# Performance work log

Hardware: AMD Instinct MI355X
Metric: run time of the kernel (lower is better)

The kernel has to match this reference:

```python
import jax, jax.numpy as jnp
import numpy as np

B, S, C, D, P = 32, 720, 2048, 256, 96
LATENT_DIMS = [512, 128, 32]  # enc_in // 4 ** k, e_layers=3
NL = 3
ALPHA = 0.1
EPS = 1e-5


def _ln(x, g, b, eps=1e-5):
    m = jnp.mean(x, axis=-1, keepdims=True)
    v = jnp.var(x, axis=-1, keepdims=True)
    return (x - m) * jax.lax.rsqrt(v + eps) * g + b


def _cov_loss(skips, lam=ALPHA, eps=EPS):
    total = jnp.zeros((), dtype=jnp.float32)
    for x in skips[1:]:
        b, c, d = x.shape
        xr = x.reshape(b * c, d)
        xc = (xr - jnp.mean(xr, axis=0, keepdims=True)) / (jnp.std(xr, axis=0, ddof=1, keepdims=True) + eps)
        cov = xc.T @ xc / (b * c - 1) + eps * jnp.eye(d, dtype=x.dtype)
        total = total - jnp.linalg.slogdet(cov)[1] / d
    return lam * total / (len(skips) - 1)


def setup_inputs() -> dict:
    key = jax.random.key(0)
    ks = jax.random.split(key, 16)
    w = lambda k, shp: (jax.random.normal(k, shp, dtype=jnp.float32) * 0.02)
    inp = {
        'x_enc': jax.random.normal(ks[0], (B, S, C), dtype=jnp.float32),
        'x_mark_enc': jnp.zeros((B, S, 4), dtype=jnp.float32),
        'x_dec': jnp.zeros((B, P, C), dtype=jnp.float32),
        'x_mark_dec': jnp.zeros((B, P, 4), dtype=jnp.float32),
        'in_w': w(ks[1], (S, D)), 'in_b': jnp.zeros((D,), jnp.float32),
        'lq0': jax.random.normal(ks[2], (LATENT_DIMS[0], D), dtype=jnp.float32),
        'lq1': jax.random.normal(ks[3], (LATENT_DIMS[1], D), dtype=jnp.float32),
        'lq2': jax.random.normal(ks[4], (LATENT_DIMS[2], D), dtype=jnp.float32),
        'down_w': w(ks[5], (NL, 4, D, D)), 'down_b': jnp.zeros((NL, 4, D), jnp.float32),
        'down_ln': jnp.stack([jnp.ones((NL, D)), jnp.zeros((NL, D))], axis=1).astype(jnp.float32),
        'pred_w': w(ks[6], (D, D)), 'pred_b': jnp.zeros((D,), jnp.float32),
        'up_w': w(ks[7], (NL, 4, D, D)), 'up_b': jnp.zeros((NL, 4, D), jnp.float32),
        'up_ln': jnp.stack([jnp.ones((NL, D)), jnp.zeros((NL, D))], axis=1).astype(jnp.float32),
        'out_w': w(ks[8], (D, P)), 'out_b': jnp.zeros((P,), jnp.float32),
    }
    return inp


def _forward(x_enc, in_w, in_b, lqs, down_w, down_b, down_ln,
             pred_w, pred_b, up_w, up_b, up_ln, out_w, out_b):
    # instance norm over time
    means = jnp.mean(x_enc, axis=1, keepdims=True)            # [B,1,C]
    xc = x_enc - means
    stdev = jnp.sqrt(jnp.var(xc, axis=1, keepdims=True) + 1e-5)
    xn = xc / stdev
    # transpose + Linear(seq_len -> d_model): [B,C,D]
    h = jnp.einsum('bsc,sd->bcd', xn, in_w) + in_b

    scale = 1.0 / jnp.sqrt(jnp.asarray(D, dtype=h.dtype))
    skips = [h]
    x = h
    for i in range(NL):
        Wq, Wk, Wv, Wo = down_w[i]
        bq, bk, bv, bo = down_b[i]
        q = lqs[i] @ Wq + bq                                  # [Lq,D] shared over batch
        k = x @ Wk + bk                                       # [B,L,D]
        v = x @ Wv + bv
        attn = jax.nn.softmax(jnp.einsum('qd,bld->bql', q, k) * scale, axis=-1)
        o = jnp.einsum('bql,bld->bqd', attn, v) @ Wo + bo
        x = _ln(o, down_ln[i, 0], down_ln[i, 1])
        skips.append(x)

    cov = _cov_loss(skips)

    x = x @ pred_w + pred_b                                   # bottom [B,32,D]
    queries = skips[::-1][1:]                                 # [128-skip, 512-skip, base]
    for i, qin in enumerate(queries):
        Wq, Wk, Wv, Wo = up_w[i]
        bq, bk, bv, bo = up_b[i]
        q = qin @ Wq + bq                                     # [B,Lq,D]
        k = x @ Wk + bk                                       # [B,Lk,D]
        v = x @ Wv + bv
        attn = jax.nn.softmax(jnp.einsum('bqd,bld->bql', q, k) * scale, axis=-1)
        o = jnp.einsum('bql,bld->bqd', attn, v) @ Wo + bo
        x = _ln(o + qin, up_ln[i, 0], up_ln[i, 1])

    dec = (x + h) @ out_w + out_b                             # [B,C,P]
    dec = jnp.transpose(dec, (0, 2, 1))                       # [B,P,C]
    dec = dec * stdev[:, 0, :][:, None, :] + means[:, 0, :][:, None, :]
    return dec, cov


def reference(x_enc, x_mark_enc, x_dec, x_mark_dec, in_w, in_b, lq0, lq1, lq2,
              down_w, down_b, down_ln, pred_w, pred_b, up_w, up_b, up_ln, out_w, out_b):
    return _forward(x_enc, in_w, in_b, (lq0, lq1, lq2), down_w, down_b, down_ln,
                    pred_w, pred_b, up_w, up_b, up_ln, out_w, out_b)
```

## Files before the change

kernel.cpp:

```cpp
#include <hip/hip_runtime.h>
#include <hip/hip_bf16.h>
#include <math.h>

#define CDIV(a, b) (((a) + (b) - 1) / (b))
typedef long long ll;
typedef unsigned short ushort_t;

constexpr int Bn = 32;
constexpr int Sn = 720;
constexpr int SnP = 736;
constexpr int Cn = 2048;
constexpr int Dn = 256;
constexpr int Pn = 96;

typedef __attribute__((ext_vector_type(8))) short bf16x8;
typedef __attribute__((ext_vector_type(4))) float f32x4;

__device__ inline ushort_t rne1(float x) {
  unsigned u = __float_as_uint(x);
  u = (u + 0x7fffu + ((u >> 16) & 1u)) >> 16;
  return (ushort_t)u;
}
__device__ inline float b2f(ushort_t u) { return __uint_as_float(((unsigned)u) << 16); }

__device__ inline void gl_lds16(const void* g, void* l) {
  __builtin_amdgcn_global_load_lds(
      (const __attribute__((address_space(1))) void*)g,
      (__attribute__((address_space(3))) void*)l, 16, 0, 0);
}

__global__ void instnorm_stats(const float* __restrict__ x,
                               float* __restrict__ mean, float* __restrict__ stdev) {
  int c = blockIdx.x * 256 + threadIdx.x;
  int b = blockIdx.y;
  const float* p = x + (ll)b * Sn * Cn + c;
  float s = 0.f, q = 0.f;
  for (int t = 0; t < Sn; ++t) {
    float v = p[(ll)t * Cn];
    s += v; q += v * v;
  }
  float m = s / (float)Sn;
  float var = q / (float)Sn - m * m;
  var = fmaxf(var, 0.f);
  mean[b * Cn + c] = m;
  stdev[b * Cn + c] = sqrtf(var + 1e-5f);
}

__global__ void normT_kernel(const float* __restrict__ X, ushort_t* __restrict__ D,
                             const float* __restrict__ mean,
                             const float* __restrict__ stdev) {
  int b = blockIdx.z;
  __shared__ float tl[32][33];
  int t = threadIdx.x;
  int tx = t & 31, ty = t >> 5;
  int s0 = blockIdx.y * 32, c0 = blockIdx.x * 32;
#pragma unroll
  for (int e = 0; e < 4; ++e) {
    int s = s0 + ty + 8 * e;
    tl[ty + 8 * e][tx] = (s < Sn) ? X[((ll)b * Sn + s) * Cn + c0 + tx] : 0.f;
  }
  __syncthreads();
#pragma unroll
  for (int e = 0; e < 4; ++e) {
    int c = c0 + ty + 8 * e, s = s0 + tx;
    if (s < SnP) {
      float mu = mean[b * Cn + c], sd = stdev[b * Cn + c];
      float v = (s < Sn) ? (tl[tx][ty + 8 * e] - mu) / sd : 0.f;
      D[((ll)b * Cn + c) * SnP + s] = rne1(v);
    }
  }
}

__global__ void cvtT_kernel(const float* __restrict__ S, ushort_t* __restrict__ D,
                            int K, int N, int KP) {
  int z = blockIdx.z;
  S += (ll)z * K * N;
  D += (ll)z * N * KP;
  __shared__ float tl[32][33];
  int t = threadIdx.x;
  int tx = t & 31, ty = t >> 5;
  int k0 = blockIdx.y * 32, n0 = blockIdx.x * 32;
#pragma unroll
  for (int e = 0; e < 4; ++e) {
    int k = k0 + ty + 8 * e;
    tl[ty + 8 * e][tx] = (k < K && n0 + tx < N) ? S[(ll)k * N + n0 + tx] : 0.f;
  }
  __syncthreads();
#pragma unroll
  for (int e = 0; e < 4; ++e) {
    int n = n0 + ty + 8 * e, kk = k0 + tx;
    if (n < N && kk < KP) D[(ll)n * KP + kk] = rne1(tl[tx][ty + 8 * e]);
  }
}

__global__ void cvt_bf(const float* __restrict__ S, ushort_t* __restrict__ D, int n) {
  int i = blockIdx.x * 256 + threadIdx.x;
  if (i < n) D[i] = rne1(S[i]);
}

template <int MODE>
__global__ __launch_bounds__(256) void gemm_bf(
    const ushort_t* __restrict__ A, const ushort_t* __restrict__ B,
    int M, int N, int K, int lda, int ldb, ll sA, ll sB,
    const float* __restrict__ bias, float alpha,
    float* __restrict__ Cf, int ldcf, ll sCf,
    ushort_t* __restrict__ Cb, int ldcb, ll sCb) {
  int g = blockIdx.z;
  A += (ll)g * sA;
  B += (ll)g * sB;
  if (MODE & 1) Cf += (ll)g * sCf;
  if (MODE & 6) Cb += (ll)g * sCb;
  __shared__ ushort_t lds_ab[2][128][32];
  int t = threadIdx.x;
  int m0 = blockIdx.y * 128, n0 = blockIdx.x * 128;
  int w = t >> 6, lane = t & 63;
  int wm = (w >> 1) * 64, wn = (w & 1) * 64;
  int lrow = lane & 15, kq = lane >> 4;
  int srow = lane >> 2, skcol = (lane & 3) * 8;
  f32x4 acc[4][4] = {};
  for (int k0 = 0; k0 < K; k0 += 32) {
#pragma unroll
    for (int cc = 0; cc < 4; ++cc) {
      int c = w * 4 + cc;
      int tile = c >> 3, rb = (c & 7) * 16;
      int row = rb + srow;
      const ushort_t* src;
      if (tile == 0) {
        int gm = min(m0 + row, M - 1);
        src = &A[(ll)gm * lda + k0 + skcol];
      } else {
        int gn = min(n0 + row, N - 1);
        src = &B[(ll)gn * ldb + k0 + skcol];
      }
      gl_lds16(src, &lds_ab[tile][rb][0]);
    }
    __syncthreads();
    bf16x8 af[4], bfr[4];
#pragma unroll
    for (int i = 0; i < 4; ++i)
      af[i] = *reinterpret_cast<const bf16x8*>(&lds_ab[0][wm + i * 16 + lrow][kq * 8]);
#pragma unroll
    for (int j = 0; j < 4; ++j)
      bfr[j] = *reinterpret_cast<const bf16x8*>(&lds_ab[1][wn + j * 16 + lrow][kq * 8]);
#pragma unroll
    for (int i = 0; i < 4; ++i)
#pragma unroll
      for (int j = 0; j < 4; ++j)
        acc[i][j] = __builtin_amdgcn_mfma_f32_16x16x32_bf16(af[i], bfr[j],
                                                            acc[i][j], 0, 0, 0);
    __syncthreads();
  }
#pragma unroll
  for (int i = 0; i < 4; ++i) {
    int mb = m0 + wm + i * 16 + kq * 4;
    if (mb >= M) continue;
#pragma unroll
    for (int j = 0; j < 4; ++j) {
      int c = n0 + wn + j * 16 + lrow;
      if (c >= N) continue;
      float bv = bias ? bias[c] : 0.f;
#pragma unroll
      for (int reg = 0; reg < 4; ++reg) {
        int m = mb + reg;
        float v = acc[i][j][reg] * alpha + bv;
        if (MODE & 1) Cf[(ll)m * ldcf + c] = v;
        if (MODE & 2) Cb[(ll)m * ldcb + c] = rne1(v);
        if (MODE & 4) Cb[(ll)c * ldcb + m] = rne1(v);
      }
    }
  }
}

__device__ inline float blk_reduce(float v, volatile float* sh, int op) {
  int lane = threadIdx.x & 63, w = threadIdx.x >> 6;
#pragma unroll
  for (int off = 32; off > 0; off >>= 1) {
    float o = __shfl_down(v, off, 64);
    v = op ? fmaxf(v, o) : (v + o);
  }
  __syncthreads();
  if (lane == 0) sh[w] = v;
  __syncthreads();
  float r = op ? fmaxf(fmaxf(sh[0], sh[1]), fmaxf(sh[2], sh[3]))
               : (sh[0] + sh[1] + sh[2] + sh[3]);
  return r;
}

template <int LL>
__global__ void softmax_bf(const float* __restrict__ S, ushort_t* __restrict__ P) {
  constexpr int NE = (LL + 255) / 256;
  __shared__ float sh[4];
  ll row = blockIdx.x;
  const float* p = S + row * (ll)LL;
  ushort_t* q = P + row * (ll)LL;
  int t = threadIdx.x;
  float e[NE];
  float mx = -INFINITY;
#pragma unroll
  for (int k = 0; k < NE; ++k) {
    int i = t + k * 256;
    if (i < LL) { e[k] = p[i]; mx = fmaxf(mx, e[k]); }
  }
  mx = blk_reduce(mx, sh, 1);
  float sum = 0.f;
#pragma unroll
  for (int k = 0; k < NE; ++k) {
    int i = t + k * 256;
    if (i < LL) { e[k] = __expf(e[k] - mx); sum += e[k]; }
  }
  sum = blk_reduce(sum, sh, 0);
  float inv = 1.f / sum;
#pragma unroll
  for (int k = 0; k < NE; ++k) {
    int i = t + k * 256;
    if (i < LL) q[i] = rne1(e[k] * inv);
  }
}

__global__ void ln_kernel(const float* __restrict__ X, const ushort_t* __restrict__ RESb,
                          float* __restrict__ Yf, ushort_t* __restrict__ Yb, int postadd,
                          const float* __restrict__ gamma, const float* __restrict__ beta) {
  __shared__ float sh[4];
  ll row = blockIdx.x;
  int t = threadIdx.x;
  float r = RESb ? b2f(RESb[row * Dn + t]) : 0.f;
  float v = X[row * Dn + t] + r;
  float m = blk_reduce(v, sh, 0) * (1.f / (float)Dn);
  float d = v - m;
  float var = blk_reduce(d * d, sh, 0) * (1.f / (float)Dn);
  float y = d * rsqrtf(var + 1e-5f) * gamma[t] + beta[t];
  if (Yf) Yf[row * Dn + t] = y;
  if (Yb) Yb[row * Dn + t] = rne1(y + (postadd ? r : 0.f));
}

__global__ void colstat_partial(const float* __restrict__ X, double* __restrict__ part,
                                int nrows) {
  int blk = blockIdx.x, t = threadIdx.x;
  int chunk = CDIV(nrows, 256);
  int r0 = blk * chunk, r1 = min(nrows, r0 + chunk);
  double s = 0.0, q = 0.0;
  for (int r = r0; r < r1; ++r) {
    double v = (double)X[(ll)r * Dn + t];
    s += v; q += v * v;
  }
  part[blk * 512 + t] = s;
  part[blk * 512 + 256 + t] = q;
}

__global__ void colstat_final(const double* __restrict__ part, float* __restrict__ cmean,
                              float* __restrict__ cistd, int nrows) {
  int t = threadIdx.x;
  double s = 0.0, q = 0.0;
  for (int b = 0; b < 256; ++b) {
    s += part[b * 512 + t];
    q += part[b * 512 + 256 + t];
  }
  double m = s / (double)nrows;
  double var = (q - (double)nrows * m * m) / (double)(nrows - 1);
  var = fmax(var, 0.0);
  cmean[t] = (float)m;
  cistd[t] = (float)(1.0 / (sqrt(var) + 1e-5));
}

__global__ __launch_bounds__(256) void cov_gram(const float* __restrict__ X,
                                                const float* __restrict__ cmean,
                                                const float* __restrict__ cistd,
                                                double* __restrict__ part, int nr) {
  __shared__ double Am[32][33];
  __shared__ double Bq[32][33];
  __shared__ float cmA[32], ciA[32], cmB[32], ciB[32];
  int tile = blockIdx.x;
  int mi = 0;
  while (tile >= mi + 1) { tile -= mi + 1; ++mi; }
  int nj = tile;
  int m0 = mi * 32, n0 = nj * 32;
  int z = blockIdx.y;
  int t = threadIdx.x, tx = t & 31, ty = t >> 5;
  if (t < 32) {
    cmA[t] = cmean[m0 + t]; ciA[t] = cistd[m0 + t];
    cmB[t] = cmean[n0 + t]; ciB[t] = cistd[n0 + t];
  }
  __syncthreads();
  int chunk = nr >> 4;
  int kbeg = z * chunk, kend = kbeg + chunk;
  double acc[4] = {0.0, 0.0, 0.0, 0.0};
  for (int k0 = kbeg; k0 < kend; k0 += 32) {
#pragma unroll
    for (int e = 0; e < 4; ++e) {
      int idx = t + e * 256;
      int kk = idx >> 5, mm = idx & 31;
      float xa = X[(ll)(k0 + kk) * Dn + m0 + mm];
      float xb = X[(ll)(k0 + kk) * Dn + n0 + mm];
      Am[kk][mm] = (double)((xa - cmA[mm]) * ciA[mm]);
      Bq[kk][mm] = (double)((xb - cmB[mm]) * ciB[mm]);
    }
    __syncthreads();
#pragma unroll 8
    for (int kk = 0; kk < 32; ++kk) {
      double bv = Bq[kk][tx];
#pragma unroll
      for (int r = 0; r < 4; ++r)
        acc[r] += Am[kk][ty + 8 * r] * bv;
    }
    __syncthreads();
  }
#pragma unroll
  for (int r = 0; r < 4; ++r) {
    int m = m0 + ty + 8 * r, n = n0 + tx;
    part[(ll)z * 65536 + m * 256 + n] = acc[r];
  }
}

__global__ void cov_reduce(const double* __restrict__ part, double* __restrict__ Cd,
                           double inv) {
  int tile = blockIdx.x;
  int mi = 0;
  while (tile >= mi + 1) { tile -= mi + 1; ++mi; }
  int nj = tile;
  int t = threadIdx.x;
#pragma unroll
  for (int e = 0; e < 4; ++e) {
    int idx = t + e * 256;
    int rr = idx >> 5, cc = idx & 31;
    int m = mi * 32 + rr, n = nj * 32 + cc;
    int off = m * 256 + n;
    double s = 0.0;
#pragma unroll
    for (int z = 0; z < 16; ++z) s += part[(ll)z * 65536 + off];
    Cd[off] = s * inv + ((m == n) ? 1e-5 : 0.0);
  }
}

__global__ __launch_bounds__(256) void chol_step_a(double* __restrict__ mats, int d0) {
  double* A = mats + (ll)blockIdx.x * 65536;
  __shared__ double D[32][33];
  __shared__ double dinv[32];
  int t = threadIdx.x;
  for (int e = t; e < 1024; e += 256) {
    int i = e >> 5, j = e & 31;
    D[i][j] = (j <= i) ? A[(ll)(d0 + i) * 256 + d0 + j] : 0.0;
  }
  __syncthreads();
  if (t < 32) {
    double x[32];
#pragma unroll
    for (int j = 0; j < 32; ++j) x[j] = D[t][j];
#pragma unroll
    for (int k = 0; k < 32; ++k) {
      double piv = fmax(__shfl(x[k], k, 64), 1e-300);
      double inv = 1.0 / sqrt(piv);
      double lrk = x[k] * inv;
      x[k] = lrk;
#pragma unroll
      for (int j = k + 1; j < 32; ++j) x[j] -= lrk * __shfl(lrk, j, 64);
    }
#pragma unroll
    for (int j = 0; j < 32; ++j) D[t][j] = x[j];
    dinv[t] = 1.0 / x[t];
  }
  __syncthreads();
  int r = d0 + 32 + t;
  if (r < 256) {
    double y[32];
#pragma unroll
    for (int j = 0; j < 32; ++j) y[j] = A[(ll)r * 256 + d0 + j];
#pragma unroll
    for (int j = 0; j < 32; ++j) {
      double s = y[j];
#pragma unroll
      for (int i = 0; i < j; ++i) s -= y[i] * D[j][i];
      y[j] = s * dinv[j];
    }
#pragma unroll
    for (int j = 0; j < 32; ++j) A[(ll)r * 256 + d0 + j] = y[j];
  }
  for (int e = t; e < 1024; e += 256)
    A[(ll)(d0 + (e >> 5)) * 256 + d0 + (e & 31)] = D[e >> 5][e & 31];
}

__global__ __launch_bounds__(256) void chol_step_b(double* __restrict__ mats, int d0) {
  double* A = mats + (ll)blockIdx.y * 65536;
  int tile = blockIdx.x;
  int i = 0;
  while (tile >= i + 1) { tile -= i + 1; ++i; }
  int j = tile;
  int ri = d0 + 32 + i * 32, rj = d0 + 32 + j * 32;
  __shared__ double Li[32][33];
  __shared__ double Lj[32][33];
  int t = threadIdx.x;
  for (int e = t; e < 1024; e += 256) {
    int rr = e >> 5, kk = e & 31;
    Li[rr][kk] = A[(ll)(ri + rr) * 256 + d0 + kk];
    Lj[rr][kk] = A[(ll)(rj + rr) * 256 + d0 + kk];
  }
  __syncthreads();
  for (int e = t; e < 1024; e += 256) {
    int rr = e >> 5, cc = e & 31;
    double s = 0.0;
#pragma unroll
    for (int k = 0; k < 32; ++k) s += Li[rr][k] * Lj[cc][k];
    A[(ll)(ri + rr) * 256 + rj + cc] -= s;
  }
}

__global__ void logdet_diag(const double* __restrict__ mats, double* __restrict__ ld) {
  __shared__ double sh[4];
  const double* A = mats + (ll)blockIdx.x * 65536;
  int t = threadIdx.x;
  double lg = log(A[(ll)t * 257]);
  int lane = t & 63, w = t >> 6;
#pragma unroll
  for (int off = 32; off > 0; off >>= 1) lg += __shfl_down(lg, off, 64);
  if (lane == 0) sh[w] = lg;
  __syncthreads();
  if (t == 0) ld[blockIdx.x] = 2.0 * (sh[0] + sh[1] + sh[2] + sh[3]);
}

__global__ void cov_final(const double* __restrict__ ld, float* __restrict__ outp) {
  outp[0] = (float)(-0.1 / (3.0 * 256.0) * (ld[0] + ld[1] + ld[2]));
}

__global__ __launch_bounds__(256) void out_mfma(
    const ushort_t* __restrict__ A, const ushort_t* __restrict__ B,
    const float* __restrict__ bias, const float* __restrict__ stdev,
    const float* __restrict__ mean, float* __restrict__ out) {
  constexpr int M = Bn * Cn, N = Pn, K = Dn;
  __shared__ ushort_t lds_ab[2][128][32];
  int t = threadIdx.x;
  int m0 = blockIdx.y * 128;
  int w = t >> 6, lane = t & 63;
  int wm = (w >> 1) * 64, wn = (w & 1) * 64;
  int lrow = lane & 15, kq = lane >> 4;
  int srow = lane >> 2, skcol = (lane & 3) * 8;
  f32x4 acc[4][4] = {};
  for (int k0 = 0; k0 < K; k0 += 32) {
#pragma unroll
    for (int cc = 0; cc < 4; ++cc) {
      int c = w * 4 + cc;
      int tile = c >> 3, rb = (c & 7) * 16;
      int row = rb + srow;
      const ushort_t* src;
      if (tile == 0) {
        src = &A[(ll)(m0 + row) * K + k0 + skcol];
      } else {
        int gn = min(row, N - 1);
        src = &B[(ll)gn * K + k0 + skcol];
      }
      gl_lds16(src, &lds_ab[tile][rb][0]);
    }
    __syncthreads();
    bf16x8 af[4], bfr[4];
#pragma unroll
    for (int i = 0; i < 4; ++i)
      af[i] = *reinterpret_cast<const bf16x8*>(&lds_ab[0][wm + i * 16 + lrow][kq * 8]);
#pragma unroll
    for (int j = 0; j < 4; ++j)
      bfr[j] = *reinterpret_cast<const bf16x8*>(&lds_ab[1][wn + j * 16 + lrow][kq * 8]);
#pragma unroll
    for (int i = 0; i < 4; ++i)
#pragma unroll
      for (int j = 0; j < 4; ++j)
        acc[i][j] = __builtin_amdgcn_mfma_f32_16x16x32_bf16(af[i], bfr[j],
                                                            acc[i][j], 0, 0, 0);
    __syncthreads();
  }
#pragma unroll
  for (int i = 0; i < 4; ++i) {
    int mb = m0 + wm + i * 16 + kq * 4;
#pragma unroll
    for (int j = 0; j < 4; ++j) {
      int p = wn + j * 16 + lrow;
      if (p >= N) continue;
      float bv = bias[p];
#pragma unroll
      for (int reg = 0; reg < 4; ++reg) {
        int m = mb + reg;
        int b = m >> 11, c = m & 2047;
        float v = acc[i][j][reg] + bv;
        out[((ll)(b * Pn + p)) * Cn + c] = v * stdev[m] + mean[m];
      }
    }
  }
}

extern "C" void kernel_launch(void* const* d_in, const int* in_sizes, int n_in,
                              void* d_out, int out_size, void* d_ws, size_t ws_size,
                              hipStream_t stream) {
  (void)in_sizes; (void)n_in; (void)out_size; (void)ws_size;
  const float* x_enc = (const float*)d_in[0];
  const float* in_w = (const float*)d_in[4];
  const float* in_b = (const float*)d_in[5];
  const float* lq[3] = {(const float*)d_in[6], (const float*)d_in[7],
                        (const float*)d_in[8]};
  const float* down_w = (const float*)d_in[9];
  const float* down_b = (const float*)d_in[10];
  const float* down_ln = (const float*)d_in[11];
  const float* pred_w = (const float*)d_in[12];
  const float* pred_b = (const float*)d_in[13];
  const float* up_w = (const float*)d_in[14];
  const float* up_b = (const float*)d_in[15];
  const float* up_ln = (const float*)d_in[16];
  const float* out_w = (const float*)d_in[17];
  const float* out_b = (const float*)d_in[18];
  float* out = (float*)d_out;

  float* ws = (float*)d_ws;
  size_t off = 0;
  auto alloc = [&](size_t n) {
    n = (n + 3) & ~(size_t)3;
    float* p = ws + off;
    off += n;
    return p;
  };
  float* mean = alloc((size_t)Bn * Cn);
  float* stdevv = alloc((size_t)Bn * Cn);
  float* cmean = alloc(256);
  float* cistd = alloc(256);
  double* part = (double*)alloc(256 * 512 * 2);
  double* ld = (double*)alloc(16);
  double* covd = (double*)alloc(3 * 65536 * 2);
  float* s1 = alloc((size_t)Bn * 512 * Dn);
  float* s2 = alloc((size_t)Bn * 128 * Dn);
  float* s3 = alloc((size_t)Bn * 32 * Dn);
  float* attn = alloc((size_t)Bn * 512 * 2048);
  float* sbuf = alloc((size_t)16777216);
  ushort_t* h_bf = (ushort_t*)alloc((size_t)Bn * Cn * Dn / 2);
  ushort_t* s1b = (ushort_t*)alloc((size_t)Bn * 512 * Dn / 2);
  ushort_t* s2b = (ushort_t*)alloc((size_t)Bn * 128 * Dn / 2);
  ushort_t* s3b = (ushort_t*)alloc((size_t)Bn * 32 * Dn / 2);
  ushort_t* xpb = (ushort_t*)alloc((size_t)Bn * 32 * Dn / 2);
  ushort_t* xu0b = (ushort_t*)alloc((size_t)Bn * 128 * Dn / 2);
  ushort_t* xu1b = (ushort_t*)alloc((size_t)Bn * 512 * Dn / 2);
  ushort_t* qd_b = (ushort_t*)alloc(512 * 256 / 2);
  ushort_t* lqb0 = (ushort_t*)alloc(512 * 256 / 2);
  ushort_t* lqb1 = (ushort_t*)alloc(128 * 256 / 2);
  ushort_t* lqb2 = (ushort_t*)alloc(32 * 256 / 2);
  ushort_t* in_wT = (ushort_t*)alloc(256 * SnP / 2);
  ushort_t* downT = (ushort_t*)alloc(12 * 65536 / 2);
  ushort_t* upT = (ushort_t*)alloc(12 * 65536 / 2);
  ushort_t* predT = (ushort_t*)alloc(65536 / 2);
  ushort_t* outT = (ushort_t*)alloc(96 * 256 / 2);
  ushort_t* q_bf = (ushort_t*)alloc((size_t)Bn * 2048 * Dn / 2);
  ushort_t* k_bf = (ushort_t*)alloc((size_t)Bn * 2048 * Dn / 2);
  ushort_t* vT = (ushort_t*)alloc((size_t)Bn * 2048 * Dn / 2);

  ushort_t* xnT = (ushort_t*)attn;
  ushort_t* attn_b = (ushort_t*)sbuf;
  float* o2 = sbuf;
  double* covpart = (double*)sbuf;
  const float scale = 0.0625f;
  const float* npf = nullptr;

  instnorm_stats<<<dim3(Cn / 256, Bn), 256, 0, stream>>>(x_enc, mean, stdevv);
  normT_kernel<<<dim3(Cn / 32, SnP / 32, Bn), 256, 0, stream>>>(x_enc, xnT, mean,
                                                                stdevv);
  cvtT_kernel<<<dim3(8, 8, 12), 256, 0, stream>>>(down_w, downT, 256, 256, 256);
  cvtT_kernel<<<dim3(8, 8, 12), 256, 0, stream>>>(up_w, upT, 256, 256, 256);
  cvtT_kernel<<<dim3(8, 8, 1), 256, 0, stream>>>(pred_w, predT, 256, 256, 256);
  cvtT_kernel<<<dim3(8, SnP / 32, 1), 256, 0, stream>>>(in_w, in_wT, Sn, 256, SnP);
  cvtT_kernel<<<dim3(3, 8, 1), 256, 0, stream>>>(out_w, outT, 256, Pn, 256);
  cvt_bf<<<512, 256, 0, stream>>>(lq[0], lqb0, 512 * 256);
  cvt_bf<<<128, 256, 0, stream>>>(lq[1], lqb1, 128 * 256);
  cvt_bf<<<32, 256, 0, stream>>>(lq[2], lqb2, 32 * 256);

  gemm_bf<2><<<dim3(2, 16, Bn), 256, 0, stream>>>(
      xnT, in_wT, Cn, Dn, SnP, SnP, SnP, (ll)Cn * SnP, 0, in_b, 1.f,
      nullptr, 0, 0, h_bf, Dn, (ll)Cn * Dn);

  ushort_t* lqb[3] = {lqb0, lqb1, lqb2};
  float* skf[3] = {s1, s2, s3};
  ushort_t* skb[3] = {s1b, s2b, s3b};
  int Ls[4] = {2048, 512, 128, 32};
  const ushort_t* xinb = h_bf;

  for (int i = 0; i < 3; ++i) {
    int L = Ls[i], Lq = Ls[i + 1];
    const ushort_t* WqT = downT + (size_t)(i * 4 + 0) * 65536;
    const ushort_t* WkT = downT + (size_t)(i * 4 + 1) * 65536;
    const ushort_t* WvT = downT + (size_t)(i * 4 + 2) * 65536;
    const ushort_t* WoT = downT + (size_t)(i * 4 + 3) * 65536;
    const float* bq = down_b + (i * 4 + 0) * 256;
    const float* bk = down_b + (i * 4 + 1) * 256;
    const float* bv = down_b + (i * 4 + 2) * 256;
    const float* bo = down_b + (i * 4 + 3) * 256;

    gemm_bf<2><<<dim3(2, CDIV(Lq, 128), 1), 256, 0, stream>>>(
        lqb[i], WqT, Lq, Dn, Dn, Dn, Dn, 0, 0, bq, 1.f, nullptr, 0, 0, qd_b, Dn, 0);
    gemm_bf<2><<<dim3(2, (Bn * L) / 128, 1), 256, 0, stream>>>(
        xinb, WkT, Bn * L, Dn, Dn, Dn, Dn, 0, 0, bk, 1.f, nullptr, 0, 0, k_bf, Dn, 0);
    gemm_bf<4><<<dim3(2, L / 128, Bn), 256, 0, stream>>>(
        xinb, WvT, L, Dn, Dn, Dn, Dn, (ll)L * Dn, 0, bv, 1.f, nullptr, 0, 0,
        vT, L, (ll)Dn * L);
    gemm_bf<1><<<dim3(L / 128, CDIV(Lq, 128), Bn), 256, 0, stream>>>(
        qd_b, k_bf, Lq, L, Dn, Dn, Dn, 0, (ll)L * Dn, npf, scale,
        attn, L, (ll)Lq * L, nullptr, 0, 0);
    if (L == 2048) softmax_bf<2048><<<Bn * Lq, 256, 0, stream>>>(attn, attn_b);
    else if (L == 512) softmax_bf<512><<<Bn * Lq, 256, 0, stream>>>(attn, attn_b);
    else softmax_bf<128><<<Bn * Lq, 256, 0, stream>>>(attn, attn_b);
    gemm_bf<2><<<dim3(2, CDIV(Lq, 128), Bn), 256, 0, stream>>>(
        attn_b, vT, Lq, Dn, L, L, L, (ll)Lq * L, (ll)Dn * L, npf, 1.f,
        nullptr, 0, 0, q_bf, Dn, (ll)Lq * Dn);
    gemm_bf<1><<<dim3(2, CDIV(Bn * Lq, 128), 1), 256, 0, stream>>>(
        q_bf, WoT, Bn * Lq, Dn, Dn, Dn, Dn, 0, 0, bo, 1.f, o2, Dn, 0, nullptr, 0, 0);
    ln_kernel<<<Bn * Lq, 256, 0, stream>>>(o2, nullptr, skf[i], skb[i], 0,
                                           down_ln + (i * 2 + 0) * 256,
                                           down_ln + (i * 2 + 1) * 256);
    xinb = skb[i];
  }

  int nrs[3] = {Bn * 512, Bn * 128, Bn * 32};
  for (int j = 0; j < 3; ++j) {
    int nr = nrs[j];
    colstat_partial<<<256, 256, 0, stream>>>(skf[j], part, nr);
    colstat_final<<<1, 256, 0, stream>>>(part, cmean, cistd, nr);
    cov_gram<<<dim3(36, 16), 256, 0, stream>>>(skf[j], cmean, cistd, covpart, nr);
    cov_reduce<<<36, 256, 0, stream>>>(covpart, covd + (size_t)j * 65536,
                                       1.0 / (double)(nr - 1));
  }
  for (int kb = 0; kb < 8; ++kb) {
    chol_step_a<<<3, 256, 0, stream>>>(covd, kb * 32);
    int T = 7 - kb;
    if (T > 0)
      chol_step_b<<<dim3(T * (T + 1) / 2, 3), 256, 0, stream>>>(covd, kb * 32);
  }
  logdet_diag<<<3, 256, 0, stream>>>(covd, ld);
  cov_final<<<1, 1, 0, stream>>>(ld, out + 6291456);

  gemm_bf<2><<<dim3(2, 8, 1), 256, 0, stream>>>(
      s3b, predT, Bn * 32, Dn, Dn, Dn, Dn, 0, 0, pred_b, 1.f,
      nullptr, 0, 0, xpb, Dn, 0);

  int Lks[3] = {32, 128, 512}, Lqs[3] = {128, 512, 2048};
  const ushort_t* qinb[3] = {s2b, s1b, h_bf};
  const ushort_t* xinbs[3] = {xpb, xu0b, xu1b};
  ushort_t* xoutb[3] = {xu0b, xu1b, q_bf};
  for (int i = 0; i < 3; ++i) {
    int Lk = Lks[i], Lq = Lqs[i];
    const ushort_t* WqT = upT + (size_t)(i * 4 + 0) * 65536;
    const ushort_t* WkT = upT + (size_t)(i * 4 + 1) * 65536;
    const ushort_t* WvT = upT + (size_t)(i * 4 + 2) * 65536;
    const ushort_t* WoT = upT + (size_t)(i * 4 + 3) * 65536;
    const float* bq = up_b + (i * 4 + 0) * 256;
    const float* bk = up_b + (i * 4 + 1) * 256;
    const float* bv = up_b + (i * 4 + 2) * 256;
    const float* bo = up_b + (i * 4 + 3) * 256;

    gemm_bf<2><<<dim3(2, (Bn * Lq) / 128, 1), 256, 0, stream>>>(
        qinb[i], WqT, Bn * Lq, Dn, Dn, Dn, Dn, 0, 0, bq, 1.f,
        nullptr, 0, 0, q_bf, Dn, 0);
    gemm_bf<2><<<dim3(2, CDIV(Bn * Lk, 128), 1), 256, 0, stream>>>(
        xinbs[i], WkT, Bn * Lk, Dn, Dn, Dn, Dn, 0, 0, bk, 1.f,
        nullptr, 0, 0, k_bf, Dn, 0);
    gemm_bf<4><<<dim3(2, CDIV(Lk, 128), Bn), 256, 0, stream>>>(
        xinbs[i], WvT, Lk, Dn, Dn, Dn, Dn, (ll)Lk * Dn, 0, bv, 1.f,
        nullptr, 0, 0, vT, Lk, (ll)Dn * Lk);
    gemm_bf<1><<<dim3(CDIV(Lk, 128), CDIV(Lq, 128), Bn), 256, 0, stream>>>(
        q_bf, k_bf, Lq, Lk, Dn, Dn, Dn, (ll)Lq * Dn, (ll)Lk * Dn, npf, scale,
        attn, Lk, (ll)Lq * Lk, nullptr, 0, 0);
    if (Lk == 32) softmax_bf<32><<<Bn * Lq, 256, 0, stream>>>(attn, attn_b);
    else if (Lk == 128) softmax_bf<128><<<Bn * Lq, 256, 0, stream>>>(attn, attn_b);
    else softmax_bf<512><<<Bn * Lq, 256, 0, stream>>>(attn, attn_b);
    gemm_bf<2><<<dim3(2, CDIV(Lq, 128), Bn), 256, 0, stream>>>(
        attn_b, vT, Lq, Dn, Lk, Lk, Lk, (ll)Lq * Lk, (ll)Dn * Lk, npf, 1.f,
        nullptr, 0, 0, q_bf, Dn, (ll)Lq * Dn);
    gemm_bf<1><<<dim3(2, (Bn * Lq) / 128, 1), 256, 0, stream>>>(
        q_bf, WoT, Bn * Lq, Dn, Dn, Dn, Dn, 0, 0, bo, 1.f, o2, Dn, 0, nullptr, 0, 0);
    ln_kernel<<<Bn * Lq, 256, 0, stream>>>(o2, qinb[i], nullptr, xoutb[i],
                                           (i == 2) ? 1 : 0,
                                           up_ln + (i * 2 + 0) * 256,
                                           up_ln + (i * 2 + 1) * 256);
  }

  out_mfma<<<dim3(1, (Bn * Cn) / 128, 1), 256, 0, stream>>>(q_bf, outT, out_b,
                                                            stdevv, mean, out);
}
```

Measured before the change: 1.854 ms.

## Fuse blocked Cholesky into one kernel and retile covariance Gram with 64x64 tiles

Replaces the 15 per-step Cholesky launches plus the logdet kernel with a single 1024-thread kernel per matrix. That kernel keeps the current panel in LDS and accumulates the log-diagonal inline. The covariance Gram kernel moves to 64x64 lower-triangle tiles with 4x4 register blocking, loads only one operand on diagonal tiles, and uses per-layer split-K counts. The goal is to cut launch overhead and LDS traffic in the small fp64 covariance/logdet path. The trade-off is that the fused Cholesky runs on only 3 blocks with a serial per-panel critical path, and the larger split-K raises partial-buffer traffic.

Measured after the change: 2.357 ms. +27.1%, slower.

```diff
diff --git a/kernel.cpp b/kernel.cpp
--- a/kernel.cpp
+++ b/kernel.cpp
@@ -265,155 +265,148 @@
 __global__ __launch_bounds__(256) void cov_gram(const float* __restrict__ X,
                                                 const float* __restrict__ cmean,
                                                 const float* __restrict__ cistd,
-                                                double* __restrict__ part, int nr) {
-  __shared__ double Am[32][33];
-  __shared__ double Bq[32][33];
-  __shared__ float cmA[32], ciA[32], cmB[32], ciB[32];
+                                                double* __restrict__ part,
+                                                int nr, int nz) {
+  __shared__ double Am[32][66];
+  __shared__ double Bq[32][66];
+  __shared__ float cmA[64], ciA[64], cmB[64], ciB[64];
   int tile = blockIdx.x;
   int mi = 0;
   while (tile >= mi + 1) { tile -= mi + 1; ++mi; }
   int nj = tile;
-  int m0 = mi * 32, n0 = nj * 32;
+  int m0 = mi * 64, n0 = nj * 64;
+  bool diag = (mi == nj);
   int z = blockIdx.y;
-  int t = threadIdx.x, tx = t & 31, ty = t >> 5;
-  if (t < 32) {
-    cmA[t] = cmean[m0 + t]; ciA[t] = cistd[m0 + t];
-    cmB[t] = cmean[n0 + t]; ciB[t] = cistd[n0 + t];
-  }
+  int t = threadIdx.x;
+  int tx4 = (t & 15) * 4, ty4 = (t >> 4) * 4;
+  if (t < 64) { cmA[t] = cmean[m0 + t]; ciA[t] = cistd[m0 + t]; }
+  else if (t < 128) { cmB[t - 64] = cmean[n0 + t - 64]; ciB[t - 64] = cistd[n0 + t - 64]; }
   __syncthreads();
-  int chunk = nr >> 4;
+  int chunk = nr / nz;
   int kbeg = z * chunk, kend = kbeg + chunk;
-  double acc[4] = {0.0, 0.0, 0.0, 0.0};
+  double acc[4][4] = {};
+  const double* Bbase = diag ? &Am[0][0] : &Bq[0][0];
   for (int k0 = kbeg; k0 < kend; k0 += 32) {
 #pragma unroll
-    for (int e = 0; e < 4; ++e) {
+    for (int e = 0; e < 8; ++e) {
       int idx = t + e * 256;
-      int kk = idx >> 5, mm = idx & 31;
+      int kk = idx >> 6, mm = idx & 63;
       float xa = X[(ll)(k0 + kk) * Dn + m0 + mm];
-      float xb = X[(ll)(k0 + kk) * Dn + n0 + mm];
       Am[kk][mm] = (double)((xa - cmA[mm]) * ciA[mm]);
-      Bq[kk][mm] = (double)((xb - cmB[mm]) * ciB[mm]);
-    }
-    __syncthreads();
-#pragma unroll 8
+      if (!diag) {
+        float xb = X[(ll)(k0 + kk) * Dn + n0 + mm];
+        Bq[kk][mm] = (double)((xb - cmB[mm]) * ciB[mm]);
+      }
+    }
+    __syncthreads();
+#pragma unroll 4
     for (int kk = 0; kk < 32; ++kk) {
-      double bv = Bq[kk][tx];
-#pragma unroll
-      for (int r = 0; r < 4; ++r)
-        acc[r] += Am[kk][ty + 8 * r] * bv;
-    }
-    __syncthreads();
-  }
-#pragma unroll
-  for (int r = 0; r < 4; ++r) {
-    int m = m0 + ty + 8 * r, n = n0 + tx;
-    part[(ll)z * 65536 + m * 256 + n] = acc[r];
-  }
+      double a[4], b[4];
+#pragma unroll
+      for (int q = 0; q < 4; ++q) a[q] = Am[kk][ty4 + q];
+#pragma unroll
+      for (int q = 0; q < 4; ++q) b[q] = Bbase[kk * 66 + tx4 + q];
+#pragma unroll
+      for (int i = 0; i < 4; ++i)
+#pragma unroll
+        for (int j = 0; j < 4; ++j) acc[i][j] += a[i] * b[j];
+    }
+    __syncthreads();
+  }
+  ll base = ((ll)z * 10 + blockIdx.x) * 4096;
+#pragma unroll
+  for (int i = 0; i < 4; ++i)
+#pragma unroll
+    for (int j = 0; j < 4; ++j)
+      part[base + (ty4 + i) * 64 + tx4 + j] = acc[i][j];
 }
 
 __global__ void cov_reduce(const double* __restrict__ part, double* __restrict__ Cd,
-                           double inv) {
+                           double inv, int nz) {
   int tile = blockIdx.x;
   int mi = 0;
   while (tile >= mi + 1) { tile -= mi + 1; ++mi; }
   int nj = tile;
   int t = threadIdx.x;
-#pragma unroll
-  for (int e = 0; e < 4; ++e) {
-    int idx = t + e * 256;
-    int rr = idx >> 5, cc = idx & 31;
-    int m = mi * 32 + rr, n = nj * 32 + cc;
-    int off = m * 256 + n;
+  for (int e = t; e < 4096; e += 256) {
+    int rr = e >> 6, cc = e & 63;
+    int m = mi * 64 + rr, n = nj * 64 + cc;
     double s = 0.0;
-#pragma unroll
-    for (int z = 0; z < 16; ++z) s += part[(ll)z * 65536 + off];
-    Cd[off] = s * inv + ((m == n) ? 1e-5 : 0.0);
-  }
-}
-
-__global__ __launch_bounds__(256) void chol_step_a(double* __restrict__ mats, int d0) {
+    for (int z = 0; z < nz; ++z) s += part[((ll)z * 10 + blockIdx.x) * 4096 + e];
+    Cd[m * 256 + n] = s * inv + ((m == n) ? 1e-5 : 0.0);
+  }
+}
+
+__global__ __launch_bounds__(1024) void cholesky_fused(double* __restrict__ mats,
+                                                       double* __restrict__ ld) {
   double* A = mats + (ll)blockIdx.x * 65536;
-  __shared__ double D[32][33];
+  __shared__ double P[256][33];
   __shared__ double dinv[32];
   int t = threadIdx.x;
-  for (int e = t; e < 1024; e += 256) {
-    int i = e >> 5, j = e & 31;
-    D[i][j] = (j <= i) ? A[(ll)(d0 + i) * 256 + d0 + j] : 0.0;
-  }
-  __syncthreads();
-  if (t < 32) {
-    double x[32];
-#pragma unroll
-    for (int j = 0; j < 32; ++j) x[j] = D[t][j];
-#pragma unroll
-    for (int k = 0; k < 32; ++k) {
-      double piv = fmax(__shfl(x[k], k, 64), 1e-300);
-      double inv = 1.0 / sqrt(piv);
-      double lrk = x[k] * inv;
-      x[k] = lrk;
-#pragma unroll
-      for (int j = k + 1; j < 32; ++j) x[j] -= lrk * __shfl(lrk, j, 64);
-    }
-#pragma unroll
-    for (int j = 0; j < 32; ++j) D[t][j] = x[j];
-    dinv[t] = 1.0 / x[t];
-  }
-  __syncthreads();
-  int r = d0 + 32 + t;
-  if (r < 256) {
-    double y[32];
-#pragma unroll
-    for (int j = 0; j < 32; ++j) y[j] = A[(ll)r * 256 + d0 + j];
-#pragma unroll
-    for (int j = 0; j < 32; ++j) {
-      double s = y[j];
-#pragma unroll
-      for (int i = 0; i < j; ++i) s -= y[i] * D[j][i];
-      y[j] = s * dinv[j];
-    }
-#pragma unroll
-    for (int j = 0; j < 32; ++j) A[(ll)r * 256 + d0 + j] = y[j];
-  }
-  for (int e = t; e < 1024; e += 256)
-    A[(ll)(d0 + (e >> 5)) * 256 + d0 + (e & 31)] = D[e >> 5][e & 31];
-}
-
-__global__ __launch_bounds__(256) void chol_step_b(double* __restrict__ mats, int d0) {
-  double* A = mats + (ll)blockIdx.y * 65536;
-  int tile = blockIdx.x;
-  int i = 0;
-  while (tile >= i + 1) { tile -= i + 1; ++i; }
-  int j = tile;
-  int ri = d0 + 32 + i * 32, rj = d0 + 32 + j * 32;
-  __shared__ double Li[32][33];
-  __shared__ double Lj[32][33];
-  int t = threadIdx.x;
-  for (int e = t; e < 1024; e += 256) {
-    int rr = e >> 5, kk = e & 31;
-    Li[rr][kk] = A[(ll)(ri + rr) * 256 + d0 + kk];
-    Lj[rr][kk] = A[(ll)(rj + rr) * 256 + d0 + kk];
-  }
-  __syncthreads();
-  for (int e = t; e < 1024; e += 256) {
-    int rr = e >> 5, cc = e & 31;
-    double s = 0.0;
-#pragma unroll
-    for (int k = 0; k < 32; ++k) s += Li[rr][k] * Lj[cc][k];
-    A[(ll)(ri + rr) * 256 + rj + cc] -= s;
-  }
-}
-
-__global__ void logdet_diag(const double* __restrict__ mats, double* __restrict__ ld) {
-  __shared__ double sh[4];
-  const double* A = mats + (ll)blockIdx.x * 65536;
-  int t = threadIdx.x;
-  double lg = log(A[(ll)t * 257]);
-  int lane = t & 63, w = t >> 6;
-#pragma unroll
-  for (int off = 32; off > 0; off >>= 1) lg += __shfl_down(lg, off, 64);
-  if (lane == 0) sh[w] = lg;
-  __syncthreads();
-  if (t == 0) ld[blockIdx.x] = 2.0 * (sh[0] + sh[1] + sh[2] + sh[3]);
+  double lsum = 0.0;
+  for (int kb = 0; kb < 8; ++kb) {
+    int d0 = kb * 32;
+    int nrows = 256 - d0;
+    for (int e = t; e < nrows * 32; e += 1024) {
+      int rr = e >> 5, j = e & 31;
+      P[d0 + rr][j] = (rr < 32 && j > rr) ? 0.0 : A[(ll)(d0 + rr) * 256 + d0 + j];
+    }
+    __syncthreads();
+    if (t < 32) {
+      double x[32];
+#pragma unroll
+      for (int j = 0; j < 32; ++j) x[j] = P[d0 + t][j];
+#pragma unroll
+      for (int k = 0; k < 32; ++k) {
+        double piv = fmax(__shfl(x[k], k, 64), 1e-300);
+        double inv = 1.0 / sqrt(piv);
+        double lrk = x[k] * inv;
+        x[k] = lrk;
+#pragma unroll
+        for (int j = k + 1; j < 32; ++j) x[j] -= lrk * __shfl(lrk, j, 64);
+      }
+#pragma unroll
+      for (int j = 0; j < 32; ++j) P[d0 + t][j] = x[j];
+      dinv[t] = 1.0 / x[t];
+      double lg = log(x[t]);
+#pragma unroll
+      for (int off = 16; off > 0; off >>= 1) lg += __shfl_down(lg, off, 32);
+      if (t == 0) lsum += lg;
+    }
+    __syncthreads();
+    int T = nrows - 32;
+    if (t < T) {
+      int r = d0 + 32 + t;
+      double y[32];
+#pragma unroll
+      for (int j = 0; j < 32; ++j) y[j] = P[r][j];
+#pragma unroll
+      for (int j = 0; j < 32; ++j) {
+        double s = y[j];
+#pragma unroll
+        for (int i = 0; i < j; ++i) s -= y[i] * P[d0 + j][i];
+        y[j] = s * dinv[j];
+      }
+#pragma unroll
+      for (int j = 0; j < 32; ++j) P[r][j] = y[j];
+    }
+    __syncthreads();
+    int total = T * (T + 1) / 2;
+    for (int e = t; e < total; e += 1024) {
+      int i = (int)((sqrtf(8.f * (float)e + 1.f) - 1.f) * 0.5f);
+      while ((i + 1) * (i + 2) / 2 <= e) ++i;
+      while (i * (i + 1) / 2 > e) --i;
+      int j = e - i * (i + 1) / 2;
+      const double* Pi = P[d0 + 32 + i];
+      const double* Pj = P[d0 + 32 + j];
+      double s = 0.0;
+#pragma unroll
+      for (int k = 0; k < 32; ++k) s += Pi[k] * Pj[k];
+      A[(ll)(d0 + 32 + i) * 256 + d0 + 32 + j] -= s;
+    }
+    __syncthreads();
+  }
+  if (t == 0) ld[blockIdx.x] = 2.0 * lsum;
 }
 
 __global__ void cov_final(const double* __restrict__ ld, float* __restrict__ outp) {
@@ -609,21 +602,17 @@
   }
 
   int nrs[3] = {Bn * 512, Bn * 128, Bn * 32};
+  int nzs[3] = {64, 32, 16};
   for (int j = 0; j < 3; ++j) {
     int nr = nrs[j];
     colstat_partial<<<256, 256, 0, stream>>>(skf[j], part, nr);
     colstat_final<<<1, 256, 0, stream>>>(part, cmean, cistd, nr);
-    cov_gram<<<dim3(36, 16), 256, 0, stream>>>(skf[j], cmean, cistd, covpart, nr);
-    cov_reduce<<<36, 256, 0, stream>>>(covpart, covd + (size_t)j * 65536,
-                                       1.0 / (double)(nr - 1));
-  }
-  for (int kb = 0; kb < 8; ++kb) {
-    chol_step_a<<<3, 256, 0, stream>>>(covd, kb * 32);
-    int T = 7 - kb;
-    if (T > 0)
-      chol_step_b<<<dim3(T * (T + 1) / 2, 3), 256, 0, stream>>>(covd, kb * 32);
-  }
-  logdet_diag<<<3, 256, 0, stream>>>(covd, ld);
+    cov_gram<<<dim3(10, nzs[j]), 256, 0, stream>>>(skf[j], cmean, cistd, covpart,
+                                                   nr, nzs[j]);
+    cov_reduce<<<10, 256, 0, stream>>>(covpart, covd + (size_t)j * 65536,
+                                       1.0 / (double)(nr - 1), nzs[j]);
+  }
+  cholesky_fused<<<3, 1024, 0, stream>>>(covd, ld);
   cov_final<<<1, 1, 0, stream>>>(ld, out + 6291456);
 
   gemm_bf<2><<<dim3(2, 8, 1), 256, 0, stream>>>(
```

## Retile covariance Gram kernel to 64x64 register-blocked tiles with adaptive split-K

Applied to the files above, without the earlier changes.

The fp64 covariance Gram kernel moves from 32x32 tiles with one output column per thread and four rows to 64x64 lower-triangular tiles where each thread computes a 4x4 register block, which raises arithmetic per shared-memory load. Diagonal tiles load a single operand and reuse it for both sides. The split-K factor now depends on the row count (64/32/16), and partials are stored in a compact per-tile layout that the reduction kernel sums. This trades fewer blocks (10 tiles per split) for more work per thread and more fp64 accumulator registers, which may lower occupancy.

New measurement: 2.257 ms. +21.7%, slower.

```diff
diff --git a/kernel.cpp b/kernel.cpp
--- a/kernel.cpp
+++ b/kernel.cpp
@@ -265,69 +265,75 @@
 __global__ __launch_bounds__(256) void cov_gram(const float* __restrict__ X,
                                                 const float* __restrict__ cmean,
                                                 const float* __restrict__ cistd,
-                                                double* __restrict__ part, int nr) {
-  __shared__ double Am[32][33];
-  __shared__ double Bq[32][33];
-  __shared__ float cmA[32], ciA[32], cmB[32], ciB[32];
+                                                double* __restrict__ part,
+                                                int nr, int nz) {
+  __shared__ double Am[32][66];
+  __shared__ double Bq[32][66];
+  __shared__ float cmA[64], ciA[64], cmB[64], ciB[64];
   int tile = blockIdx.x;
   int mi = 0;
   while (tile >= mi + 1) { tile -= mi + 1; ++mi; }
   int nj = tile;
-  int m0 = mi * 32, n0 = nj * 32;
+  int m0 = mi * 64, n0 = nj * 64;
+  bool diag = (mi == nj);
   int z = blockIdx.y;
-  int t = threadIdx.x, tx = t & 31, ty = t >> 5;
-  if (t < 32) {
-    cmA[t] = cmean[m0 + t]; ciA[t] = cistd[m0 + t];
-    cmB[t] = cmean[n0 + t]; ciB[t] = cistd[n0 + t];
-  }
-  __syncthreads();
-  int chunk = nr >> 4;
+  int t = threadIdx.x;
+  int tx4 = (t & 15) * 4, ty4 = (t >> 4) * 4;
+  if (t < 64) { cmA[t] = cmean[m0 + t]; ciA[t] = cistd[m0 + t]; }
+  else if (t < 128) { cmB[t - 64] = cmean[n0 + t - 64]; ciB[t - 64] = cistd[n0 + t - 64]; }
+  __syncthreads();
+  int chunk = nr / nz;
   int kbeg = z * chunk, kend = kbeg + chunk;
-  double acc[4] = {0.0, 0.0, 0.0, 0.0};
+  double acc[4][4] = {};
+  const double* Bbase = diag ? &Am[0][0] : &Bq[0][0];
   for (int k0 = kbeg; k0 < kend; k0 += 32) {
 #pragma unroll
-    for (int e = 0; e < 4; ++e) {
+    for (int e = 0; e < 8; ++e) {
       int idx = t + e * 256;
-      int kk = idx >> 5, mm = idx & 31;
+      int kk = idx >> 6, mm = idx & 63;
       float xa = X[(ll)(k0 + kk) * Dn + m0 + mm];
-      float xb = X[(ll)(k0 + kk) * Dn + n0 + mm];
       Am[kk][mm] = (double)((xa - cmA[mm]) * ciA[mm]);
-      Bq[kk][mm] = (double)((xb - cmB[mm]) * ciB[mm]);
+      if (!diag) {
+        float xb = X[(ll)(k0 + kk) * Dn + n0 + mm];
+        Bq[kk][mm] = (double)((xb - cmB[mm]) * ciB[mm]);
+      }
     }
     __syncthreads();
-#pragma unroll 8
+#pragma unroll 4
     for (int kk = 0; kk < 32; ++kk) {
-      double bv = Bq[kk][tx];
-#pragma unroll
-      for (int r = 0; r < 4; ++r)
-        acc[r] += Am[kk][ty + 8 * r] * bv;
+      double a[4], b[4];
+#pragma unroll
+      for (int q = 0; q < 4; ++q) a[q] = Am[kk][ty4 + q];
+#pragma unroll
+      for (int q = 0; q < 4; ++q) b[q] = Bbase[kk * 66 + tx4 + q];
+#pragma unroll
+      for (int i = 0; i < 4; ++i)
+#pragma unroll
+        for (int j = 0; j < 4; ++j) acc[i][j] += a[i] * b[j];
     }
     __syncthreads();
   }
-#pragma unroll
-  for (int r = 0; r < 4; ++r) {
-    int m = m0 + ty + 8 * r, n = n0 + tx;
-    part[(ll)z * 65536 + m * 256 + n] = acc[r];
-  }
+  ll base = ((ll)z * 10 + blockIdx.x) * 4096;
+#pragma unroll
+  for (int i = 0; i < 4; ++i)
+#pragma unroll
+    for (int j = 0; j < 4; ++j)
+      part[base + (ty4 + i) * 64 + tx4 + j] = acc[i][j];
 }
 
 __global__ void cov_reduce(const double* __restrict__ part, double* __restrict__ Cd,
-                           double inv) {
+                           double inv, int nz) {
   int tile = blockIdx.x;
   int mi = 0;
   while (tile >= mi + 1) { tile -= mi + 1; ++mi; }
   int nj = tile;
   int t = threadIdx.x;
-#pragma unroll
-  for (int e = 0; e < 4; ++e) {
-    int idx = t + e * 256;
-    int rr = idx >> 5, cc = idx & 31;
-    int m = mi * 32 + rr, n = nj * 32 + cc;
-    int off = m * 256 + n;
+  for (int e = t; e < 4096; e += 256) {
+    int rr = e >> 6, cc = e & 63;
+    int m = mi * 64 + rr, n = nj * 64 + cc;
     double s = 0.0;
-#pragma unroll
-    for (int z = 0; z < 16; ++z) s += part[(ll)z * 65536 + off];
-    Cd[off] = s * inv + ((m == n) ? 1e-5 : 0.0);
+    for (int z = 0; z < nz; ++z) s += part[((ll)z * 10 + blockIdx.x) * 4096 + e];
+    Cd[m * 256 + n] = s * inv + ((m == n) ? 1e-5 : 0.0);
   }
 }
 
@@ -517,7 +523,7 @@
   float* cmean = alloc(256);
   float* cistd = alloc(256);
   double* part = (double*)alloc(256 * 512 * 2);
-  double* ld = (double*)alloc(16);
+  double* ld = (double*)alloc(32);
   double* covd = (double*)alloc(3 * 65536 * 2);
   float* s1 = alloc((size_t)Bn * 512 * Dn);
   float* s2 = alloc((size_t)Bn * 128 * Dn);
@@ -609,13 +615,15 @@
   }
 
   int nrs[3] = {Bn * 512, Bn * 128, Bn * 32};
+  int nzs[3] = {64, 32, 16};
   for (int j = 0; j < 3; ++j) {
     int nr = nrs[j];
     colstat_partial<<<256, 256, 0, stream>>>(skf[j], part, nr);
     colstat_final<<<1, 256, 0, stream>>>(part, cmean, cistd, nr);
-    cov_gram<<<dim3(36, 16), 256, 0, stream>>>(skf[j], cmean, cistd, covpart, nr);
-    cov_reduce<<<36, 256, 0, stream>>>(covpart, covd + (size_t)j * 65536,
-                                       1.0 / (double)(nr - 1));
+    cov_gram<<<dim3(10, nzs[j]), 256, 0, stream>>>(skf[j], cmean, cistd, covpart,
+                                                   nr, nzs[j]);
+    cov_reduce<<<10, 256, 0, stream>>>(covpart, covd + (size_t)j * 65536,
+                                       1.0 / (double)(nr - 1), nzs[j]);
   }
   for (int kb = 0; kb < 8; ++kb) {
     chol_step_a<<<3, 256, 0, stream>>>(covd, kb * 32);
```
